# Optimization experiments

Hardware: AMD Instinct MI355X
Metric: run time of the kernel (lower is better)

Reference implementation:

```python
import jax, jax.numpy as jnp
import numpy as np

N_HEAD = 16
ROPE_BASE = 10000.0


def _make_rope(max_seq, half_dim):
    inv_freq = 1.0 / (ROPE_BASE ** (np.arange(0, half_dim, dtype=np.float32) / half_dim))
    t = np.arange(max_seq, dtype=np.float32)
    freqs = np.outer(t, inv_freq)  # [T, half_dim]
    return jnp.asarray(np.cos(freqs)), jnp.asarray(np.sin(freqs))


def setup_inputs() -> dict:
    key = jax.random.key(0)
    k1, k2, k3 = jax.random.split(key, 3)
    B, T, C = 4, 2048, 2048
    D = C // N_HEAD
    x = jax.random.normal(k1, (B, T, C), dtype=jnp.float32)
    # torch Linear weight [out,in]; stored transposed so y = x @ W
    wqkv = jax.random.normal(k2, (C, 3 * C), dtype=jnp.float32) * (C ** -0.5)
    wo = jax.random.normal(k3, (C, C), dtype=jnp.float32) * (C ** -0.5)
    rope_cos, rope_sin = _make_rope(T, D // 2)
    return {"x": x, "wqkv": wqkv, "wo": wo, "rope_cos": rope_cos, "rope_sin": rope_sin}


def _apply_rope(t, cos, sin):
    # t: [B, T, H, D]; cos/sin: [T, D/2]
    B, T, H, D = t.shape
    tr = t.reshape(B, T, H, D // 2, 2)
    xr, xi = tr[..., 0], tr[..., 1]
    c = cos[:T][None, :, None, :]
    s = sin[:T][None, :, None, :]
    out_r = xr * c - xi * s
    out_i = xr * s + xi * c
    return jnp.stack([out_r, out_i], axis=-1).reshape(B, T, H, D)


def reference(x, wqkv, wo, rope_cos, rope_sin):
    B, T, C = x.shape
    H = N_HEAD
    D = C // H
    qkv = x @ wqkv  # [B, T, 3C]
    q, k, v = jnp.split(qkv, 3, axis=-1)
    q = _apply_rope(q.reshape(B, T, H, D), rope_cos, rope_sin)
    k = _apply_rope(k.reshape(B, T, H, D), rope_cos, rope_sin)
    v = v.reshape(B, T, H, D)
    scale = D ** -0.5
    scores = jnp.einsum('bqhd,bkhd->bhqk', q, k) * scale  # [B, H, T, T]
    causal = jnp.tril(jnp.ones((T, T), dtype=bool))
    scores = jnp.where(causal[None, None], scores, jnp.finfo(scores.dtype).min)
    attn = jax.nn.softmax(scores, axis=-1)
    y = jnp.einsum('bhqk,bkhd->bqhd', attn, v).reshape(B, T, C)
    return y @ wo
```

## Files before the change

kernel.cpp:

```cpp
#include <hip/hip_runtime.h>
#include <hip/hip_bf16.h>

typedef __attribute__((ext_vector_type(8))) __bf16 bf16x8;
typedef __attribute__((ext_vector_type(4))) float f32x4;
typedef __attribute__((ext_vector_type(4))) unsigned short us4;

__device__ __forceinline__ unsigned short f2bf(float f) {
    unsigned u = __float_as_uint(f);
    u += 0x7FFFu + ((u >> 16) & 1u);
    return (unsigned short)(u >> 16);
}

__device__ __forceinline__ void gload16(const void* g, void* l) {
    __builtin_amdgcn_global_load_lds(
        (const __attribute__((address_space(1))) unsigned int*)g,
        (__attribute__((address_space(3))) unsigned int*)l,
        16, 0, 0);
}

__global__ void cvt_f32_bf16(const float* __restrict__ in, unsigned short* __restrict__ out, int n4) {
    int i = blockIdx.x * blockDim.x + threadIdx.x;
    if (i >= n4) return;
    float4 v = ((const float4*)in)[i];
    us4 r = { f2bf(v.x), f2bf(v.y), f2bf(v.z), f2bf(v.w) };
    ((us4*)out)[i] = r;
}

__global__ void tcvt(const float* __restrict__ in, unsigned short* __restrict__ out, int R, int C) {
    __shared__ float tile[32][33];
    int tx = threadIdx.x & 31, ty = threadIdx.x >> 5;
    int c0 = blockIdx.x * 32, r0 = blockIdx.y * 32;
    #pragma unroll
    for (int i = 0; i < 32; i += 8)
        tile[ty + i][tx] = in[(size_t)(r0 + ty + i) * C + c0 + tx];
    __syncthreads();
    #pragma unroll
    for (int i = 0; i < 32; i += 8)
        out[(size_t)(c0 + ty + i) * R + r0 + tx] = f2bf(tile[tx][ty + i]);
}

#define MF(af, bf, fi, ni) acc[fi][ni] = __builtin_amdgcn_mfma_f32_16x16x32_bf16(af, bf, acc[fi][ni], 0, 0, 0)
#define LOADA(p, off) do { a0 = *(const bf16x8*)((p)+(off)); a1 = *(const bf16x8*)((p)+(off)+1024); \
                           a2 = *(const bf16x8*)((p)+(off)+2048); a3 = *(const bf16x8*)((p)+(off)+3072); } while(0)
#define LOADB(p) do { b0 = *(const bf16x8*)(p); b1 = *(const bf16x8*)((p)+1024); \
                      b2 = *(const bf16x8*)((p)+2048); b3 = *(const bf16x8*)((p)+3072); } while(0)
#define MFMA16(base) do { \
    MF(a0,b0,(base)+0,0); MF(a0,b1,(base)+0,1); MF(a0,b2,(base)+0,2); MF(a0,b3,(base)+0,3); \
    MF(a1,b0,(base)+1,0); MF(a1,b1,(base)+1,1); MF(a1,b2,(base)+1,2); MF(a1,b3,(base)+1,3); \
    MF(a2,b0,(base)+2,0); MF(a2,b1,(base)+2,1); MF(a2,b2,(base)+2,2); MF(a2,b3,(base)+2,3); \
    MF(a3,b0,(base)+3,0); MF(a3,b1,(base)+3,1); MF(a3,b2,(base)+3,2); MF(a3,b3,(base)+3,3); } while(0)
#define STG(gb, lp, buf, kkk, kt) do { \
    size_t ko = (size_t)(kt) * 128 + (kkk) * 64; \
    char* lpp = (lp) + (buf) * 32768 + (kkk) * 16384; \
    gload16((gb) + sR0 + ko, lpp + dst0); \
    gload16((gb) + sR1 + ko, lpp + dst1); } while (0)
#define PHASE_SYNC() do { \
    __builtin_amdgcn_s_barrier(); \
    asm volatile("s_waitcnt lgkmcnt(0)" ::: "memory"); \
    __builtin_amdgcn_sched_barrier(0); } while (0)

template <int MODE>
__global__ __launch_bounds__(512) void gemm8p(
    const unsigned short* __restrict__ A, const unsigned short* __restrict__ Bt,
    int M, int N, int K, float* __restrict__ Cf,
    unsigned short* __restrict__ qp, unsigned short* __restrict__ kp,
    unsigned short* __restrict__ vTp,
    const float* __restrict__ ropeC, const float* __restrict__ ropeS,
    int cby, int cbx)
{
    __shared__ unsigned short lA[2][2][8192];
    __shared__ unsigned short lB[2][2][8192];
    const int tid = threadIdx.x;
    const int lane = tid & 63, wid = tid >> 6;
    const int ln15 = lane & 15, hig = lane >> 4;
    const int wr = wid >> 2, wc = wid & 3;

    int nwg = gridDim.x * gridDim.y;
    int flat = blockIdx.y * gridDim.x + blockIdx.x;
    int bx, by;
    if ((nwg & 7) == 0) {
        int c = flat & 7, local = flat >> 3;
        int chunkCols = gridDim.x / cbx;
        by = (c / chunkCols) * cby + local / cbx;
        bx = (c % chunkCols) * cbx + local % cbx;
    } else {
        bx = flat % gridDim.x; by = flat / gridDim.x;
    }
    const int mbase = by * 256, nbase = bx * 256;
    const size_t Kb = (size_t)K * 2;

    const char* Ag = (const char*)A + (size_t)mbase * Kb;
    const char* Bg = (const char*)Bt + (size_t)nbase * Kb;
    char* lAc = (char*)&lA[0][0][0];
    char* lBc = (char*)&lB[0][0][0];

    const int srow = tid >> 2;
    const int gsrc = (tid & 3) ^ (((tid >> 5) & 1) << 1);
    const size_t sR0 = (size_t)srow * Kb + gsrc * 16;
    const size_t sR1 = (size_t)(srow + 128) * Kb + gsrc * 16;
    const int dst0 = tid * 16, dst1 = (tid + 512) * 16;

    const int colOff = (hig * 16) ^ (((ln15 >> 3) & 1) << 5);
    const int aRow = (wr * 128 + ln15) * 64 + colOff;
    const int bRow = (wc * 64 + ln15) * 64 + colOff;

    f32x4 acc[8][4] = {};
    const int T = K >> 6;

    STG(Ag, lAc, 0, 0, 0);
    STG(Bg, lBc, 0, 0, 0);
    STG(Ag, lAc, 0, 1, 0);
    STG(Bg, lBc, 0, 1, 0);
    STG(Ag, lAc, 1, 0, 1);
    STG(Bg, lBc, 1, 0, 1);
    asm volatile("s_waitcnt vmcnt(8)" ::: "memory");
    __builtin_amdgcn_s_barrier();

    for (int t = 0; t < T; t++) {
        const int cur = t & 1, nxt = cur ^ 1;
        const char* pa0 = lAc + cur * 32768 + aRow;
        const char* pb0 = lBc + cur * 32768 + bRow;
        const char* pa1 = pa0 + 16384;
        const char* pb1 = pb0 + 16384;
        const bool tail = (t >= T - 2);
        bf16x8 a0, a1, a2, a3, b0, b1, b2, b3;

        LOADA(pa0, 0);
        LOADB(pb0);
        if (t + 1 < T) STG(Ag, lAc, nxt, 1, t + 1);
        PHASE_SYNC();
        __builtin_amdgcn_s_setprio(1);
        MFMA16(0);
        __builtin_amdgcn_s_setprio(0);
        __builtin_amdgcn_s_barrier();

        LOADA(pa0, 4096);
        if (t + 1 < T) STG(Bg, lBc, nxt, 1, t + 1);
        if (tail) asm volatile("s_waitcnt vmcnt(0)" ::: "memory");
        else      asm volatile("s_waitcnt vmcnt(6)" ::: "memory");
        PHASE_SYNC();
        __builtin_amdgcn_s_setprio(1);
        MFMA16(4);
        __builtin_amdgcn_s_setprio(0);
        __builtin_amdgcn_s_barrier();

        LOADA(pa1, 0);
        LOADB(pb1);
        if (t + 2 < T) STG(Ag, lAc, cur, 0, t + 2);
        PHASE_SYNC();
        __builtin_amdgcn_s_setprio(1);
        MFMA16(0);
        __builtin_amdgcn_s_setprio(0);
        __builtin_amdgcn_s_barrier();

        LOADA(pa1, 4096);
        if (t + 2 < T) STG(Bg, lBc, cur, 0, t + 2);
        if (tail) asm volatile("s_waitcnt vmcnt(0)" ::: "memory");
        else      asm volatile("s_waitcnt vmcnt(6)" ::: "memory");
        PHASE_SYNC();
        __builtin_amdgcn_s_setprio(1);
        MFMA16(4);
        __builtin_amdgcn_s_setprio(0);
        __builtin_amdgcn_s_barrier();
    }

    if (MODE == 0) {
        #pragma unroll
        for (int fg = 0; fg < 8; fg++)
            #pragma unroll
            for (int n = 0; n < 4; n++)
                #pragma unroll
                for (int j = 0; j < 4; j++) {
                    int m = mbase + wr * 128 + fg * 16 + hig * 4 + j;
                    int col = nbase + wc * 64 + n * 16 + ln15;
                    Cf[(size_t)m * N + col] = acc[fg][n][j];
                }
    } else {
        const int colb = nbase + wc * 64;
        const int sec = colb >> 11;
        if (sec < 2) {
            unsigned short* dst = (sec == 0) ? qp : kp;
            const float scale = (sec == 0) ? 0.08838834764831845f : 1.0f;
            #pragma unroll
            for (int fg = 0; fg < 8; fg++)
                #pragma unroll
                for (int n = 0; n < 4; n++) {
                    int within = (colb & 2047) + n * 16 + ln15;
                    int h = within >> 7, d = within & 127, pidx = d >> 1;
                    #pragma unroll
                    for (int j = 0; j < 4; j++) {
                        int m = mbase + wr * 128 + fg * 16 + hig * 4 + j;
                        int b = m >> 11, tq = m & 2047;
                        float v = acc[fg][n][j];
                        float pv = __shfl_xor(v, 1);
                        float c = ropeC[tq * 64 + pidx], s = ropeS[tq * 64 + pidx];
                        float o = (d & 1) ? fmaf(pv, s, v * c) : fmaf(-pv, s, v * c);
                        o *= scale;
                        dst[((size_t)((b << 4) + h) * 2048 + tq) * 128 + d] = f2bf(o);
                    }
                }
        } else {
            #pragma unroll
            for (int fg = 0; fg < 8; fg++)
                #pragma unroll
                for (int n = 0; n < 4; n++) {
                    int within = (colb & 2047) + n * 16 + ln15;
                    int h = within >> 7, d = within & 127;
                    int m0 = mbase + wr * 128 + fg * 16 + hig * 4;
                    int b = m0 >> 11, t0 = m0 & 2047;
                    us4 pk = { f2bf(acc[fg][n][0]), f2bf(acc[fg][n][1]),
                               f2bf(acc[fg][n][2]), f2bf(acc[fg][n][3]) };
                    *(us4*)(vTp + ((size_t)((b << 4) + h) * 128 + d) * 2048 + t0) = pk;
                }
        }
    }
}

__global__ __launch_bounds__(256, 2) void attn_fwd(
    const unsigned short* __restrict__ q, const unsigned short* __restrict__ k,
    const unsigned short* __restrict__ vT, unsigned short* __restrict__ outp)
{
    __shared__ unsigned short lK[2][64 * 128];
    __shared__ unsigned short lV[2][128 * 64];
    __shared__ unsigned short lP[4 * 32 * 64];
    const int tid = threadIdx.x;
    const int lane = tid & 63, wid = tid >> 6;
    const int ln15 = lane & 15, hig = lane >> 4, hi8 = hig * 8;
    const int bh = blockIdx.x;

    const char* qg = (const char*)(q + (size_t)bh * 2048 * 128);
    const char* kg = (const char*)(k + (size_t)bh * 2048 * 128);
    const char* vg = (const char*)(vT + (size_t)bh * 128 * 2048);
    char* lKc = (char*)&lK[0][0];
    char* lVc = (char*)&lV[0][0];
    char* lPc = (char*)lP + wid * (32 * 64 * 2);
    const int b = bh >> 4, h = bh & 15;

    for (int rep = 0; rep < 2; rep++) {
        const int qt = rep == 0 ? (int)blockIdx.y : 15 - (int)blockIdx.y;
        const int qbase = qt * 128;
        const int qw = qbase + wid * 32;

        bf16x8 qf[2][4];
        #pragma unroll
        for (int mt = 0; mt < 2; mt++)
            #pragma unroll
            for (int ks = 0; ks < 4; ks++)
                qf[mt][ks] = *(const bf16x8*)(qg + ((size_t)(qw + mt * 16 + ln15) * 128 + ks * 32 + hi8) * 2);

        f32x4 o[2][8] = {};
        float mreg[2] = { -1e30f, -1e30f };
        float lreg[2] = { 0.f, 0.f };

        auto stageKV = [&](int bf, int kv0) {
            #pragma unroll
            for (int i = 0; i < 4; i++) {
                int slot = tid + i * 256;
                int row = slot >> 4, c = (slot & 15) * 16;
                gload16(kg + (size_t)(kv0 + row) * 256 + (c ^ ((row & 7) << 4)),
                        lKc + bf * 16384 + slot * 16);
            }
            #pragma unroll
            for (int i = 0; i < 4; i++) {
                int slot = tid + i * 256;
                int d = slot >> 3, c = (slot & 7) * 16;
                gload16(vg + (size_t)d * 4096 + (size_t)kv0 * 2 + (c ^ ((d & 7) << 4)),
                        lVc + bf * 16384 + slot * 16);
            }
        };

        const int ntiles = (qbase >> 6) + 2;
        stageKV(0, 0);
        if (ntiles > 1) stageKV(1, 64);

        for (int it = 0; it < ntiles; it++) {
            const int kv0 = it * 64;
            const int buf = it & 1;
            if (it + 1 < ntiles) asm volatile("s_waitcnt vmcnt(8)" ::: "memory");
            else                 asm volatile("s_waitcnt vmcnt(0)" ::: "memory");
            __builtin_amdgcn_s_barrier();

            if (kv0 <= qw + 31) {
                const char* lKb = lKc + buf * 16384;
                const char* lVb = lVc + buf * 16384;

                f32x4 s[2][4] = {};
                #pragma unroll
                for (int ks = 0; ks < 4; ks++) {
                    bf16x8 kf[4];
                    #pragma unroll
                    for (int nt = 0; nt < 4; nt++) {
                        int row = nt * 16 + ln15;
                        kf[nt] = *(const bf16x8*)(lKb + row * 256 + (((ks * 32 + hi8) * 2) ^ ((row & 7) << 4)));
                    }
                    __builtin_amdgcn_s_setprio(1);
                    #pragma unroll
                    for (int mt = 0; mt < 2; mt++)
                        #pragma unroll
                        for (int nt = 0; nt < 4; nt++)
                            s[mt][nt] = __builtin_amdgcn_mfma_f32_16x16x32_bf16(kf[nt], qf[mt][ks], s[mt][nt], 0, 0, 0);
                    __builtin_amdgcn_s_setprio(0);
                }

                if (kv0 + 63 > qw) {
                    #pragma unroll
                    for (int mt = 0; mt < 2; mt++) {
                        int qi = qw + mt * 16 + ln15;
                        #pragma unroll
                        for (int nt = 0; nt < 4; nt++)
                            #pragma unroll
                            for (int j = 0; j < 4; j++) {
                                int kvi = kv0 + nt * 16 + 4 * hig + j;
                                if (kvi > qi) s[mt][nt][j] = -1e30f;
                            }
                    }
                }

                float vmax[2];
                #pragma unroll
                for (int mt = 0; mt < 2; mt++) {
                    float v = fmaxf(fmaxf(s[mt][0][0], s[mt][0][1]), fmaxf(s[mt][0][2], s[mt][0][3]));
                    #pragma unroll
                    for (int nt = 1; nt < 4; nt++)
                        v = fmaxf(v, fmaxf(fmaxf(s[mt][nt][0], s[mt][nt][1]), fmaxf(s[mt][nt][2], s[mt][nt][3])));
                    v = fmaxf(v, __shfl_xor(v, 16));
                    v = fmaxf(v, __shfl_xor(v, 32));
                    vmax[mt] = v;
                }
                bool grow = (vmax[0] > mreg[0] + 8.0f) || (vmax[1] > mreg[1] + 8.0f);
                if (__any(grow)) {
                    float sc[2];
                    #pragma unroll
                    for (int mt = 0; mt < 2; mt++) {
                        float mn = fmaxf(mreg[mt], vmax[mt]);
                        sc[mt] = __expf(mreg[mt] - mn);
                        mreg[mt] = mn;
                        lreg[mt] *= sc[mt];
                    }
                    #pragma unroll
                    for (int mt = 0; mt < 2; mt++)
                        #pragma unroll
                        for (int j = 0; j < 4; j++) {
                            float scj = __shfl(sc[mt], 4 * hig + j);
                            #pragma unroll
                            for (int ntd = 0; ntd < 8; ntd++) o[mt][ntd][j] *= scj;
                        }
                }
                #pragma unroll
                for (int mt = 0; mt < 2; mt++) {
                    float rs = 0.f;
                    #pragma unroll
                    for (int nt = 0; nt < 4; nt++)
                        #pragma unroll
                        for (int j = 0; j < 4; j++) {
                            float p = __expf(s[mt][nt][j] - mreg[mt]);
                            s[mt][nt][j] = p;
                            rs += p;
                        }
                    rs += __shfl_xor(rs, 16);
                    rs += __shfl_xor(rs, 32);
                    lreg[mt] += rs;
                }

                #pragma unroll
                for (int mt = 0; mt < 2; mt++) {
                    int rr = mt * 16 + ln15;
                    int rx = (rr & 7) << 4;
                    #pragma unroll
                    for (int nt = 0; nt < 4; nt++) {
                        us4 pk = { f2bf(s[mt][nt][0]), f2bf(s[mt][nt][1]),
                                   f2bf(s[mt][nt][2]), f2bf(s[mt][nt][3]) };
                        int addr = rr * 128 + ((nt * 32 + hig * 8) ^ rx);
                        *(us4*)(lPc + addr) = pk;
                    }
                }

                #pragma unroll
                for (int ks2 = 0; ks2 < 2; ks2++) {
                    bf16x8 pf[2];
                    #pragma unroll
                    for (int mt = 0; mt < 2; mt++) {
                        int row = mt * 16 + ln15;
                        pf[mt] = *(const bf16x8*)(lPc + row * 128 + (((ks2 * 32 + hi8) * 2) ^ ((row & 7) << 4)));
                    }
                    #pragma unroll
                    for (int ntd = 0; ntd < 8; ntd++) {
                        int drow = ntd * 16 + ln15;
                        bf16x8 vf = *(const bf16x8*)(lVb + drow * 128 + (((ks2 * 32 + hi8) * 2) ^ ((drow & 7) << 4)));
                        __builtin_amdgcn_s_setprio(1);
                        #pragma unroll
                        for (int mt = 0; mt < 2; mt++)
                            o[mt][ntd] = __builtin_amdgcn_mfma_f32_16x16x32_bf16(pf[mt], vf, o[mt][ntd], 0, 0, 0);
                        __builtin_amdgcn_s_setprio(0);
                    }
                }
            }

            __builtin_amdgcn_s_barrier();
            if (it + 2 < ntiles) stageKV(buf, kv0 + 128);
        }

        #pragma unroll
        for (int mt = 0; mt < 2; mt++)
            #pragma unroll
            for (int j = 0; j < 4; j++) {
                float inv = 1.0f / __shfl(lreg[mt], 4 * hig + j);
                int t = qw + mt * 16 + hig * 4 + j;
                #pragma unroll
                for (int ntd = 0; ntd < 8; ntd++) {
                    int d = ntd * 16 + ln15;
                    outp[((size_t)b * 2048 + t) * 2048 + h * 128 + d] = f2bf(o[mt][ntd][j] * inv);
                }
            }
    }
}

extern "C" void kernel_launch(void* const* d_in, const int* in_sizes, int n_in,
                              void* d_out, int out_size, void* d_ws, size_t ws_size,
                              hipStream_t stream) {
    const float* x     = (const float*)d_in[0];
    const float* wqkv  = (const float*)d_in[1];
    const float* wo    = (const float*)d_in[2];
    const float* ropeC = (const float*)d_in[3];
    const float* ropeS = (const float*)d_in[4];
    float* out = (float*)d_out;
    char* ws = (char*)d_ws;
    const size_t MB = 1024 * 1024;
    unsigned short* xb    = (unsigned short*)(ws);
    unsigned short* wqkvT = (unsigned short*)(ws + 32 * MB);
    unsigned short* woT   = (unsigned short*)(ws + 56 * MB);
    unsigned short* qb    = (unsigned short*)(ws + 64 * MB);
    unsigned short* kb    = (unsigned short*)(ws + 96 * MB);
    unsigned short* vTb   = (unsigned short*)(ws + 128 * MB);
    unsigned short* attnb = (unsigned short*)(ws + 160 * MB);

    cvt_f32_bf16<<<16384, 256, 0, stream>>>(x, xb, 4194304);
    tcvt<<<dim3(192, 64), 256, 0, stream>>>(wqkv, wqkvT, 2048, 6144);
    tcvt<<<dim3(64, 64), 256, 0, stream>>>(wo, woT, 2048, 2048);
    gemm8p<1><<<dim3(24, 32), 512, 0, stream>>>(xb, wqkvT, 8192, 6144, 2048,
                                                nullptr, qb, kb, vTb, ropeC, ropeS, 8, 12);
    attn_fwd<<<dim3(64, 8), 256, 0, stream>>>(qb, kb, vTb, attnb);
    gemm8p<0><<<dim3(8, 32), 512, 0, stream>>>(attnb, woT, 8192, 2048, 2048,
                                               out, nullptr, nullptr, nullptr, nullptr, nullptr, 4, 8);
}
```

Before: 434.2 us.

## Restructure GEMM main loop into two 32-MFMA phases with one-step prefetch

Replaces the four-phase main loop of the bf16 GEMM (16 MFMAs per phase, prefetch two k-halves ahead) with two phases of 32 MFMAs each. Each phase loads all eight A fragments and four B fragments, then issues the next tile's global-to-LDS loads one step ahead. This halves the number of barriers and phase syncs per K step, which should improve MFMA density. The cost is a shallower prefetch distance, more live VGPRs for the extra A fragments, and reliance on hand-tuned waitcnt values that could expose memory latency.

```diff
diff --git a/kernel.cpp b/kernel.cpp
--- a/kernel.cpp
+++ b/kernel.cpp
@@ -42,13 +42,19 @@
 #define MF(af, bf, fi, ni) acc[fi][ni] = __builtin_amdgcn_mfma_f32_16x16x32_bf16(af, bf, acc[fi][ni], 0, 0, 0)
 #define LOADA(p, off) do { a0 = *(const bf16x8*)((p)+(off)); a1 = *(const bf16x8*)((p)+(off)+1024); \
                            a2 = *(const bf16x8*)((p)+(off)+2048); a3 = *(const bf16x8*)((p)+(off)+3072); } while(0)
+#define LOADA2(p, off) do { a4 = *(const bf16x8*)((p)+(off)); a5 = *(const bf16x8*)((p)+(off)+1024); \
+                            a6 = *(const bf16x8*)((p)+(off)+2048); a7 = *(const bf16x8*)((p)+(off)+3072); } while(0)
 #define LOADB(p) do { b0 = *(const bf16x8*)(p); b1 = *(const bf16x8*)((p)+1024); \
                       b2 = *(const bf16x8*)((p)+2048); b3 = *(const bf16x8*)((p)+3072); } while(0)
-#define MFMA16(base) do { \
-    MF(a0,b0,(base)+0,0); MF(a0,b1,(base)+0,1); MF(a0,b2,(base)+0,2); MF(a0,b3,(base)+0,3); \
-    MF(a1,b0,(base)+1,0); MF(a1,b1,(base)+1,1); MF(a1,b2,(base)+1,2); MF(a1,b3,(base)+1,3); \
-    MF(a2,b0,(base)+2,0); MF(a2,b1,(base)+2,1); MF(a2,b2,(base)+2,2); MF(a2,b3,(base)+2,3); \
-    MF(a3,b0,(base)+3,0); MF(a3,b1,(base)+3,1); MF(a3,b2,(base)+3,2); MF(a3,b3,(base)+3,3); } while(0)
+#define MFMA32() do { \
+    MF(a0,b0,0,0); MF(a0,b1,0,1); MF(a0,b2,0,2); MF(a0,b3,0,3); \
+    MF(a1,b0,1,0); MF(a1,b1,1,1); MF(a1,b2,1,2); MF(a1,b3,1,3); \
+    MF(a2,b0,2,0); MF(a2,b1,2,1); MF(a2,b2,2,2); MF(a2,b3,2,3); \
+    MF(a3,b0,3,0); MF(a3,b1,3,1); MF(a3,b2,3,2); MF(a3,b3,3,3); \
+    MF(a4,b0,4,0); MF(a4,b1,4,1); MF(a4,b2,4,2); MF(a4,b3,4,3); \
+    MF(a5,b0,5,0); MF(a5,b1,5,1); MF(a5,b2,5,2); MF(a5,b3,5,3); \
+    MF(a6,b0,6,0); MF(a6,b1,6,1); MF(a6,b2,6,2); MF(a6,b3,6,3); \
+    MF(a7,b0,7,0); MF(a7,b1,7,1); MF(a7,b2,7,2); MF(a7,b3,7,3); } while(0)
 #define STG(gb, lp, buf, kkk, kt) do { \
     size_t ko = (size_t)(kt) * 128 + (kkk) * 64; \
     char* lpp = (lp) + (buf) * 32768 + (kkk) * 16384; \
@@ -111,9 +117,7 @@
     STG(Bg, lBc, 0, 0, 0);
     STG(Ag, lAc, 0, 1, 0);
     STG(Bg, lBc, 0, 1, 0);
-    STG(Ag, lAc, 1, 0, 1);
-    STG(Bg, lBc, 1, 0, 1);
-    asm volatile("s_waitcnt vmcnt(8)" ::: "memory");
+    asm volatile("s_waitcnt vmcnt(4)" ::: "memory");
     __builtin_amdgcn_s_barrier();
 
     for (int t = 0; t < T; t++) {
@@ -122,44 +126,34 @@
         const char* pb0 = lBc + cur * 32768 + bRow;
         const char* pa1 = pa0 + 16384;
         const char* pb1 = pb0 + 16384;
-        const bool tail = (t >= T - 2);
-        bf16x8 a0, a1, a2, a3, b0, b1, b2, b3;
+        const bool more = (t + 1 < T);
+        bf16x8 a0, a1, a2, a3, a4, a5, a6, a7, b0, b1, b2, b3;
 
         LOADA(pa0, 0);
+        LOADA2(pa0, 4096);
         LOADB(pb0);
-        if (t + 1 < T) STG(Ag, lAc, nxt, 1, t + 1);
+        if (more) { STG(Ag, lAc, nxt, 0, t + 1); STG(Bg, lBc, nxt, 0, t + 1); }
+        asm volatile("s_waitcnt lgkmcnt(8)" ::: "memory");
+        if (more) asm volatile("s_waitcnt vmcnt(4)" ::: "memory");
+        else      asm volatile("s_waitcnt vmcnt(0)" ::: "memory");
         PHASE_SYNC();
         __builtin_amdgcn_s_setprio(1);
-        MFMA16(0);
+        MFMA32();
         __builtin_amdgcn_s_setprio(0);
         __builtin_amdgcn_s_barrier();
 
-        LOADA(pa0, 4096);
-        if (t + 1 < T) STG(Bg, lBc, nxt, 1, t + 1);
-        if (tail) asm volatile("s_waitcnt vmcnt(0)" ::: "memory");
-        else      asm volatile("s_waitcnt vmcnt(6)" ::: "memory");
+        LOADA(pa1, 0);
+        LOADA2(pa1, 4096);
+        LOADB(pb1);
+        if (more) {
+            STG(Ag, lAc, nxt, 1, t + 1);
+            STG(Bg, lBc, nxt, 1, t + 1);
+            asm volatile("s_waitcnt lgkmcnt(8)" ::: "memory");
+            asm volatile("s_waitcnt vmcnt(4)" ::: "memory");
+        }
         PHASE_SYNC();
         __builtin_amdgcn_s_setprio(1);
-        MFMA16(4);
-        __builtin_amdgcn_s_setprio(0);
-        __builtin_amdgcn_s_barrier();
-
-        LOADA(pa1, 0);
-        LOADB(pb1);
-        if (t + 2 < T) STG(Ag, lAc, cur, 0, t + 2);
-        PHASE_SYNC();
-        __builtin_amdgcn_s_setprio(1);
-        MFMA16(0);
-        __builtin_amdgcn_s_setprio(0);
-        __builtin_amdgcn_s_barrier();
-
-        LOADA(pa1, 4096);
-        if (t + 2 < T) STG(Bg, lBc, cur, 0, t + 2);
-        if (tail) asm volatile("s_waitcnt vmcnt(0)" ::: "memory");
-        else      asm volatile("s_waitcnt vmcnt(6)" ::: "memory");
-        PHASE_SYNC();
-        __builtin_amdgcn_s_setprio(1);
-        MFMA16(4);
+        MFMA32();
         __builtin_amdgcn_s_setprio(0);
         __builtin_amdgcn_s_barrier();
     }
```

After: 421.4 us. 2.9% less time.
